# Kernel tuning notes

Hardware: AMD Instinct MI355X
Metric: run time of the kernel (lower is better)

Reference implementation:

```python
import jax, jax.numpy as jnp
import numpy as np

N_NODES = 100000
N_EDGES = 3200000
N_GRAPHS = 512
F_IN = 35
F_OUT = 128


def setup_inputs() -> dict:
    key = jax.random.key(0)
    ks = jax.random.split(key, 16)
    x = jax.random.normal(ks[0], (N_NODES, F_IN), dtype=jnp.float32)
    edge_index = jax.random.randint(ks[1], (2, N_EDGES), 0, N_NODES, dtype=jnp.int32)
    batch = jnp.sort(jax.random.randint(ks[2], (N_NODES,), 0, N_GRAPHS, dtype=jnp.int32))
    def lin(k, fin, fout):
        s = 1.0 / np.sqrt(fin)
        return jax.random.uniform(k, (fin, fout), jnp.float32, -s, s)
    return {
        "x": x, "edge_index": edge_index, "batch": batch,
        # SAGEConv 1 (35 -> 35): lin_l acts on aggregated neighbors (has bias), lin_r on root (no bias)
        "Wl1": lin(ks[3], F_IN, F_IN), "bl1": jnp.zeros((F_IN,), jnp.float32), "Wr1": lin(ks[4], F_IN, F_IN),
        # SAGEConv 2 (35 -> 128)
        "Wl2": lin(ks[5], F_IN, F_OUT), "bl2": jnp.zeros((F_OUT,), jnp.float32), "Wr2": lin(ks[6], F_IN, F_OUT),
        # FC head
        "Wg1": lin(ks[7], F_OUT, F_OUT), "bg1": jnp.zeros((F_OUT,), jnp.float32),
        "Wg2": lin(ks[8], F_OUT, F_OUT), "bg2": jnp.zeros((F_OUT,), jnp.float32),
        "Wo": lin(ks[9], F_OUT, 1), "bo": jnp.zeros((1,), jnp.float32),
    }


def _sage_conv(x, src, dst, Wl, bl, Wr):
    # mean aggregation over incoming edges (src -> dst), PyG SAGEConv default
    msg = x[src]                                               # [E, F] gather
    s = jax.ops.segment_sum(msg, dst, num_segments=N_NODES)    # [N, F]
    cnt = jax.ops.segment_sum(jnp.ones((src.shape[0],), x.dtype), dst, num_segments=N_NODES)
    agg = s / jnp.maximum(cnt, 1.0)[:, None]
    return agg @ Wl + bl + x @ Wr


def reference(x, edge_index, batch, Wl1, bl1, Wr1, Wl2, bl2, Wr2, Wg1, bg1, Wg2, bg2, Wo, bo):
    src, dst = edge_index[0], edge_index[1]
    h = _sage_conv(x, src, dst, Wl1, bl1, Wr1)   # [N, 35]
    h = jax.nn.relu(h)
    h = _sage_conv(h, src, dst, Wl2, bl2, Wr2)   # [N, 128]
    # global max pool over each graph in the batch
    g = jax.ops.segment_max(h, batch, num_segments=N_GRAPHS)  # [G, 128]
    g = jax.nn.relu(g @ Wg1 + bg1)
    g = jax.nn.relu(g @ Wg2 + bg2)
    return g @ Wo + bo                            # [G, 1]
```

## Files before the change

kernel.cpp:

```cpp
#include <hip/hip_runtime.h>
#include <hip/hip_bf16.h>
#include <math.h>

#define FIN 35
#define FOUT 128
#define NGRAPHS 512
#define PWA 32
#define PWB 4
#define RP 36
#define STRIP1 64
#define CHUNK 8192
#define MAXBUCK 512
#define MAXBE 12288

#define STRIPM 64
#define HROW 130
#define NFRAG 48

typedef _Float16 half8 __attribute__((ext_vector_type(8)));
typedef _Float16 half4 __attribute__((ext_vector_type(4)));
typedef float f32x4 __attribute__((ext_vector_type(4)));

__device__ __forceinline__ unsigned int enc_f32(float f) {
    unsigned int u = __float_as_uint(f);
    return (u & 0x80000000u) ? ~u : (u | 0x80000000u);
}
__device__ __forceinline__ float dec_f32(unsigned int u) {
    unsigned int b = (u & 0x80000000u) ? (u ^ 0x80000000u) : ~u;
    return __uint_as_float(b);
}


__global__ __launch_bounds__(256) void hist1_kernel(const int* __restrict__ dst,
                                                    int* __restrict__ counts,
                                                    int E, int nblk1, int nbuck) {
    __shared__ int h[MAXBUCK];
    for (int t = threadIdx.x; t < nbuck; t += 256) h[t] = 0;
    __syncthreads();
    int base = blockIdx.x * CHUNK;
    int end = min(base + CHUNK, E);
    for (int e = base + threadIdx.x; e < end; e += 256)
        atomicAdd(&h[dst[e] >> 8], 1);
    __syncthreads();
    for (int t = threadIdx.x; t < nbuck; t += 256)
        counts[t * nblk1 + blockIdx.x] = h[t];
}

__global__ void partial_reduce_kernel(const int* __restrict__ v_in, int* __restrict__ partial, int SC) {
    int i = blockIdx.x * 256 + threadIdx.x;
    int v = (i < SC) ? v_in[i] : 0;
    #pragma unroll
    for (int off = 32; off > 0; off >>= 1) v += __shfl_down(v, off, 64);
    __shared__ int w[4];
    if ((threadIdx.x & 63) == 0) w[threadIdx.x >> 6] = v;
    __syncthreads();
    if (threadIdx.x == 0) partial[blockIdx.x] = w[0] + w[1] + w[2] + w[3];
}

__global__ void scan_partials_kernel(int* __restrict__ partial, int NB) {
    __shared__ int lds[1024];
    int t = threadIdx.x;
    int v = (t < NB) ? partial[t] : 0;
    lds[t] = v;
    __syncthreads();
    for (int off = 1; off < 1024; off <<= 1) {
        int tv = (t >= off) ? lds[t - off] : 0;
        __syncthreads();
        lds[t] += tv;
        __syncthreads();
    }
    if (t < NB) partial[t] = lds[t] - v;
}

__global__ void scan_final_kernel(const int* __restrict__ v_in, const int* __restrict__ partial,
                                  int* __restrict__ outx, int SC) {
    __shared__ int lds[256];
    int i = blockIdx.x * 256 + threadIdx.x;
    int v = (i < SC) ? v_in[i] : 0;
    lds[threadIdx.x] = v;
    __syncthreads();
    for (int off = 1; off < 256; off <<= 1) {
        int tv = (threadIdx.x >= off) ? lds[threadIdx.x - off] : 0;
        __syncthreads();
        lds[threadIdx.x] += tv;
        __syncthreads();
    }
    int excl = lds[threadIdx.x] - v + partial[blockIdx.x];
    if (i < SC) {
        outx[i] = excl;
        if (i == SC - 1) outx[SC] = excl + v;
    }
}

__global__ __launch_bounds__(256) void scatter1_kernel(const int* __restrict__ src,
                                                       const int* __restrict__ dst,
                                                       const int* __restrict__ offs,
                                                       int* __restrict__ ebuf,
                                                       int E, int nblk1, int nbuck) {
    __shared__ int hist[MAXBUCK];
    __shared__ int scn[256];
    __shared__ int lstart[MAXBUCK];
    __shared__ int gofs[MAXBUCK];
    __shared__ int cur[MAXBUCK];
    __shared__ int sv[CHUNK];
    __shared__ int sd[CHUNK];
    int t = threadIdx.x;
    int base = blockIdx.x * CHUNK;
    int end = min(base + CHUNK, E);

    hist[t] = 0; hist[t + 256] = 0;
    __syncthreads();
    for (int e = base + t; e < end; e += 256)
        atomicAdd(&hist[dst[e] >> 8], 1);
    __syncthreads();

    int v0 = hist[2 * t];
    int v1 = hist[2 * t + 1];
    int pair = v0 + v1;
    scn[t] = pair;
    __syncthreads();
    for (int off = 1; off < 256; off <<= 1) {
        int tv = (t >= off) ? scn[t - off] : 0;
        __syncthreads();
        scn[t] += tv;
        __syncthreads();
    }
    int ex = scn[t] - pair;
    lstart[2 * t] = ex;
    lstart[2 * t + 1] = ex + v0;
    cur[2 * t] = ex;
    cur[2 * t + 1] = ex + v0;
    int b0 = 2 * t, b1 = 2 * t + 1;
    gofs[b0] = ((b0 < nbuck) ? offs[b0 * nblk1 + blockIdx.x] : 0) - ex;
    gofs[b1] = ((b1 < nbuck) ? offs[b1 * nblk1 + blockIdx.x] : 0) - (ex + v0);
    __syncthreads();

    for (int e = base + t; e < end; e += 256) {
        int d = dst[e];
        int b = d >> 8;
        int p = atomicAdd(&cur[b], 1);
        sv[p] = (src[e] << 8) | (d & 255);
        sd[p] = gofs[b] + p;
    }
    __syncthreads();

    int cnt = end - base;
    for (int k = t; k < cnt; k += 256)
        ebuf[sd[k]] = sv[k];
}

__global__ __launch_bounds__(256) void csr2_kernel(const int* __restrict__ ebuf,
                                                   const int* __restrict__ offs,
                                                   int* __restrict__ row_ptr,
                                                   int* __restrict__ hsplit,
                                                   int* __restrict__ esrc,
                                                   int E, int nblk1, int nbuck, int N, int halfN) {
    __shared__ int h[512];
    __shared__ int scn[256];
    __shared__ int cur[512];
    __shared__ int e_sh[MAXBE];
    int b = blockIdx.x;
    int t = threadIdx.x;
    int bstart = offs[b * nblk1];
    int bend = (b + 1 < nbuck) ? offs[(b + 1) * nblk1] : E;
    int cnt = bend - bstart;
    bool fit = (cnt <= MAXBE);

    if (fit)
        for (int k = t; k < cnt; k += 256) e_sh[k] = ebuf[bstart + k];
    h[t] = 0; h[t + 256] = 0;
    __syncthreads();
    for (int k = t; k < cnt; k += 256) {
        int e = fit ? e_sh[k] : ebuf[bstart + k];
        int bin = ((e & 255) << 1) | ((e >> 8) >= halfN ? 1 : 0);
        atomicAdd(&h[bin], 1);
    }
    __syncthreads();

    int v0 = h[2 * t];
    int v1 = h[2 * t + 1];
    int pair = v0 + v1;
    scn[t] = pair;
    __syncthreads();
    for (int off = 1; off < 256; off <<= 1) {
        int tv = (t >= off) ? scn[t - off] : 0;
        __syncthreads();
        scn[t] += tv;
        __syncthreads();
    }
    int base = bstart + scn[t] - pair;
    int node = (b << 8) + t;
    if (node < N) {
        row_ptr[node] = base;
        hsplit[node] = base + v0;
    }
    if (b == 0 && t == 0) row_ptr[N] = E;
    cur[2 * t] = base;
    cur[2 * t + 1] = base + v0;
    __syncthreads();

    for (int k = t; k < cnt; k += 256) {
        int e = fit ? e_sh[k] : ebuf[bstart + k];
        int bin = ((e & 255) << 1) | ((e >> 8) >= halfN ? 1 : 0);
        int p = atomicAdd(&cur[bin], 1);
        esrc[p] = e >> 8;
    }
}

__global__ void repack_kernel(const float* __restrict__ x,
                              _Float16* __restrict__ xA, _Float16* __restrict__ xB, int N) {
    int t = blockIdx.x * 256 + threadIdx.x;
    int NA = N * PWA;
    if (t < NA) {
        int n = t >> 5;
        int f = t & 31;
        xA[t] = (_Float16)x[(long long)n * FIN + f];
    } else if (t < NA + N * PWB) {
        int c = t - NA;
        int n = c >> 2;
        int f3 = c & 3;
        float v = (f3 < 3) ? x[(long long)n * FIN + 32 + f3] : 0.0f;
        xB[c] = (_Float16)v;
    }
}

__global__ __launch_bounds__(256) void gather2_kernel(const _Float16* __restrict__ pA,
                                                      const _Float16* __restrict__ pB,
                                                      const int* __restrict__ row_ptr,
                                                      const int* __restrict__ hsplit,
                                                      const int* __restrict__ esrc,
                                                      float* __restrict__ spA,
                                                      float* __restrict__ spB,
                                                      int N, int Wtot, int WS) {
    int q = blockIdx.x & 7;
    int m = blockIdx.x >> 3;
    int w = q * WS + m * 256 + threadIdx.x;
    int wend = min((q + 1) * WS, Wtot);
    if (w >= wend) return;
    int NI = N * 4;
    int pass = w / NI;
    int t = w - pass * NI;
    int n = t >> 2;
    int quad = t & 3;
    int b = (pass == 0) ? row_ptr[n] : hsplit[n];
    int e = (pass == 0) ? hsplit[n] : row_ptr[n + 1];
    const _Float16* base = pA + (quad << 3);
    const bool doB = (quad == 0);

    float a[8] = {0,0,0,0,0,0,0,0};
    float bb[4] = {0,0,0,0};
    int k = b;
    for (; k + 8 <= e; k += 8) {
        int s0 = esrc[k],     s1 = esrc[k + 1], s2 = esrc[k + 2], s3 = esrc[k + 3];
        int s4 = esrc[k + 4], s5 = esrc[k + 5], s6 = esrc[k + 6], s7 = esrc[k + 7];
        half8 v0 = *(const half8*)(base + ((long long)s0 << 5));
        half8 v1 = *(const half8*)(base + ((long long)s1 << 5));
        half8 v2 = *(const half8*)(base + ((long long)s2 << 5));
        half8 v3 = *(const half8*)(base + ((long long)s3 << 5));
        half8 v4 = *(const half8*)(base + ((long long)s4 << 5));
        half8 v5 = *(const half8*)(base + ((long long)s5 << 5));
        half8 v6 = *(const half8*)(base + ((long long)s6 << 5));
        half8 v7 = *(const half8*)(base + ((long long)s7 << 5));
        if (doB) {
            half4 u0 = *(const half4*)(pB + ((long long)s0 << 2));
            half4 u1 = *(const half4*)(pB + ((long long)s1 << 2));
            half4 u2 = *(const half4*)(pB + ((long long)s2 << 2));
            half4 u3 = *(const half4*)(pB + ((long long)s3 << 2));
            half4 u4 = *(const half4*)(pB + ((long long)s4 << 2));
            half4 u5 = *(const half4*)(pB + ((long long)s5 << 2));
            half4 u6 = *(const half4*)(pB + ((long long)s6 << 2));
            half4 u7 = *(const half4*)(pB + ((long long)s7 << 2));
            #pragma unroll
            for (int i = 0; i < 4; ++i) {
                float p01 = (float)u0[i] + (float)u1[i];
                float p23 = (float)u2[i] + (float)u3[i];
                float p45 = (float)u4[i] + (float)u5[i];
                float p67 = (float)u6[i] + (float)u7[i];
                bb[i] += (p01 + p23) + (p45 + p67);
            }
        }
        #pragma unroll
        for (int i = 0; i < 8; ++i) {
            float p01 = (float)v0[i] + (float)v1[i];
            float p23 = (float)v2[i] + (float)v3[i];
            float p45 = (float)v4[i] + (float)v5[i];
            float p67 = (float)v6[i] + (float)v7[i];
            a[i] += (p01 + p23) + (p45 + p67);
        }
    }
    for (; k < e; ++k) {
        int s = esrc[k];
        half8 v = *(const half8*)(base + ((long long)s << 5));
        if (doB) {
            half4 u = *(const half4*)(pB + ((long long)s << 2));
            #pragma unroll
            for (int i = 0; i < 4; ++i) bb[i] += (float)u[i];
        }
        #pragma unroll
        for (int i = 0; i < 8; ++i) a[i] += (float)v[i];
    }

    float* outp = spA + ((long long)pass * N + n) * PWA + (quad << 3);
    float4 r0, r1;
    r0.x = a[0]; r0.y = a[1]; r0.z = a[2]; r0.w = a[3];
    r1.x = a[4]; r1.y = a[5]; r1.z = a[6]; r1.w = a[7];
    *(float4*)outp = r0;
    *(float4*)(outp + 4) = r1;
    if (doB) {
        float4 r;
        r.x = bb[0]; r.y = bb[1]; r.z = bb[2]; r.w = bb[3];
        *(float4*)(spB + (((long long)pass * N + n) << 2)) = r;
    }
}

__global__ __launch_bounds__(256) void nu1_kernel(const float* __restrict__ x,
                                                  const float* __restrict__ spA,
                                                  const float* __restrict__ spB,
                                                  const int* __restrict__ row_ptr,
                                                  const float* __restrict__ Wl,
                                                  const float* __restrict__ bl,
                                                  const float* __restrict__ Wr,
                                                  _Float16* __restrict__ h1A,
                                                  _Float16* __restrict__ h1B,
                                                  int N) {
    __shared__ float x_sh[STRIP1 * RP];
    __shared__ float s_sh[STRIP1 * RP];
    __shared__ int deg_sh[STRIP1];

    int node0 = blockIdx.x * STRIP1;
    if (node0 >= N) return;
    int nn = min(STRIP1, N - node0);
    int tot = nn * FIN;

    for (int t = threadIdx.x; t < STRIP1; t += 256) {
        x_sh[t * RP + 35] = 0.0f;
        s_sh[t * RP + 35] = 0.0f;
    }
    if (threadIdx.x < nn)
        deg_sh[threadIdx.x] = row_ptr[node0 + threadIdx.x + 1] - row_ptr[node0 + threadIdx.x];
    for (int t = threadIdx.x; t < tot; t += 256) {
        int nl = t / FIN;
        int i = t - nl * FIN;
        long long node = node0 + nl;
        x_sh[nl * RP + i] = x[node * FIN + i];
        float sv = (i < 32) ? (spA[node * PWA + i] + spA[((long long)N + node) * PWA + i])
                            : (spB[(node << 2) + (i - 32)] + spB[(((long long)N + node) << 2) + (i - 32)]);
        s_sh[nl * RP + i] = sv;
    }
    __syncthreads();

    int wave = threadIdx.x >> 6;
    int j = threadIdx.x & 63;
    if (j >= FIN) return;

    float wl[36], wr[36];
    #pragma unroll
    for (int i = 0; i < FIN; ++i) {
        wl[i] = Wl[i * FIN + j];
        wr[i] = Wr[i * FIN + j];
    }
    wl[35] = 0.0f; wr[35] = 0.0f;
    float blj = bl[j];

    int nstart = wave * 16;
    int nend = min(nstart + 16, nn);
    for (int nl = nstart; nl < nend; ++nl) {
        float accS = 0.0f;
        float accX = blj;
        #pragma unroll
        for (int c = 0; c < 9; ++c) {
            float4 sv = *(const float4*)&s_sh[nl * RP + 4 * c];
            float4 xv = *(const float4*)&x_sh[nl * RP + 4 * c];
            accS = fmaf(sv.x, wl[4 * c],     accS);
            accS = fmaf(sv.y, wl[4 * c + 1], accS);
            accS = fmaf(sv.z, wl[4 * c + 2], accS);
            accS = fmaf(sv.w, wl[4 * c + 3], accS);
            accX = fmaf(xv.x, wr[4 * c],     accX);
            accX = fmaf(xv.y, wr[4 * c + 1], accX);
            accX = fmaf(xv.z, wr[4 * c + 2], accX);
            accX = fmaf(xv.w, wr[4 * c + 3], accX);
        }
        float inv = 1.0f / (float)max(deg_sh[nl], 1);
        float acc = fmaxf(fmaf(accS, inv, accX), 0.0f);
        long long node = node0 + nl;
        if (j < 32) {
            h1A[(node << 5) + j] = (_Float16)acc;
        } else {
            h1B[(node << 2) + (j - 32)] = (_Float16)acc;
            if (j == 34) h1B[(node << 2) + 3] = (_Float16)0.0f;
        }
    }
}

__global__ void wprep2_kernel(const float* __restrict__ Wl, const float* __restrict__ Wr,
                              _Float16* __restrict__ wfrag) {
    int f = blockIdx.x;
    int l = threadIdx.x;
    int ps = f / 24;
    int rem = f % 24;
    int ks = rem >> 3;
    int nt = rem & 7;
    int n = nt * 16 + (l & 15);
    int kb = ks * 32 + ((l >> 4) << 3);
    half8 o;
    #pragma unroll
    for (int e = 0; e < 8; ++e) {
        int k = kb + e;
        float v = 0.0f;
        if (k < 35) v = Wl[k * FOUT + n];
        else if (k >= 36 && k < 71) v = Wr[(k - 36) * FOUT + n];
        _Float16 hi = (_Float16)v;
        o[e] = ps ? (_Float16)(v - (float)hi) : hi;
    }
    *(half8*)(wfrag + ((size_t)f * 64 + l) * 8) = o;
}

__global__ __launch_bounds__(256) void nu2_pool_mfma_kernel(const _Float16* __restrict__ h1A,
                                                            const _Float16* __restrict__ h1B,
                                                            const float* __restrict__ spA,
                                                            const float* __restrict__ spB,
                                                            const int* __restrict__ row_ptr,
                                                            const _Float16* __restrict__ wfrag,
                                                            const float* __restrict__ bl,
                                                            const int* __restrict__ batch,
                                                            unsigned int* __restrict__ genc,
                                                            int N) {
    __shared__ __align__(16) float h_sh[STRIPM * HROW];
    __shared__ int b_sh[STRIPM];

    int node0 = blockIdx.x * STRIPM;
    if (node0 >= N) return;
    int nn = min(STRIPM, N - node0);

    char* Ab = (char*)h_sh;
    const int t = threadIdx.x;
    const int lane = t & 63;
    const int wv = t >> 6;

    {
        const int r = lane;
        const long long node = (long long)node0 + r;
        const bool valid = (r < nn);
        const int sw = r & 7;
        char* rowp = Ab + r * 256;

        if (wv == 0) {
            int dg = 1;
            if (valid) dg = row_ptr[node + 1] - row_ptr[node];
            float inv = 1.0f / (float)max(dg, 1);
            #pragma unroll
            for (int u = 0; u < 3; ++u) {
                half8 h = {0,0,0,0,0,0,0,0};
                if (valid) {
                    const float* p = spA + node * 32 + u * 8;
                    const float* q = spA + ((long long)N + node) * 32 + u * 8;
                    float4 p0 = *(const float4*)p;
                    float4 p1 = *(const float4*)(p + 4);
                    float4 q0 = *(const float4*)q;
                    float4 q1 = *(const float4*)(q + 4);
                    h[0] = (_Float16)((p0.x + q0.x) * inv);
                    h[1] = (_Float16)((p0.y + q0.y) * inv);
                    h[2] = (_Float16)((p0.z + q0.z) * inv);
                    h[3] = (_Float16)((p0.w + q0.w) * inv);
                    h[4] = (_Float16)((p1.x + q1.x) * inv);
                    h[5] = (_Float16)((p1.y + q1.y) * inv);
                    h[6] = (_Float16)((p1.z + q1.z) * inv);
                    h[7] = (_Float16)((p1.w + q1.w) * inv);
                }
                *(half8*)(rowp + ((u ^ sw) << 4)) = h;
            }
        } else if (wv == 1) {
            int dg = 1;
            if (valid) dg = row_ptr[node + 1] - row_ptr[node];
            float inv = 1.0f / (float)max(dg, 1);
            half8 h3 = {0,0,0,0,0,0,0,0};
            half8 h4 = {0,0,0,0,0,0,0,0};
            half8 h5 = {0,0,0,0,0,0,0,0};
            if (valid) {
                const float* p = spA + node * 32 + 24;
                const float* q = spA + ((long long)N + node) * 32 + 24;
                float4 p0 = *(const float4*)p;
                float4 p1 = *(const float4*)(p + 4);
                float4 q0 = *(const float4*)q;
                float4 q1 = *(const float4*)(q + 4);
                h3[0] = (_Float16)((p0.x + q0.x) * inv);
                h3[1] = (_Float16)((p0.y + q0.y) * inv);
                h3[2] = (_Float16)((p0.z + q0.z) * inv);
                h3[3] = (_Float16)((p0.w + q0.w) * inv);
                h3[4] = (_Float16)((p1.x + q1.x) * inv);
                h3[5] = (_Float16)((p1.y + q1.y) * inv);
                h3[6] = (_Float16)((p1.z + q1.z) * inv);
                h3[7] = (_Float16)((p1.w + q1.w) * inv);
                float4 sb0 = *(const float4*)(spB + (node << 2));
                float4 sb1 = *(const float4*)(spB + (((long long)N + node) << 2));
                half4 ha = *(const half4*)(h1A + (node << 5));
                h4[0] = (_Float16)((sb0.x + sb1.x) * inv);
                h4[1] = (_Float16)((sb0.y + sb1.y) * inv);
                h4[2] = (_Float16)((sb0.z + sb1.z) * inv);
                h4[3] = (_Float16)((sb0.w + sb1.w) * inv);
                h4[4] = ha[0]; h4[5] = ha[1]; h4[6] = ha[2]; h4[7] = ha[3];
                half4 hb0 = *(const half4*)(h1A + (node << 5) + 4);
                half4 hb1 = *(const half4*)(h1A + (node << 5) + 8);
                h5[0] = hb0[0]; h5[1] = hb0[1]; h5[2] = hb0[2]; h5[3] = hb0[3];
                h5[4] = hb1[0]; h5[5] = hb1[1]; h5[6] = hb1[2]; h5[7] = hb1[3];
            }
            *(half8*)(rowp + ((3 ^ sw) << 4)) = h3;
            *(half8*)(rowp + ((4 ^ sw) << 4)) = h4;
            *(half8*)(rowp + ((5 ^ sw) << 4)) = h5;
        } else if (wv == 2) {
            half8 h6 = {0,0,0,0,0,0,0,0};
            half8 h7 = {0,0,0,0,0,0,0,0};
            half8 h8 = {0,0,0,0,0,0,0,0};
            if (valid) {
                half4 a0 = *(const half4*)(h1A + (node << 5) + 12);
                half4 a1 = *(const half4*)(h1A + (node << 5) + 16);
                half4 a2 = *(const half4*)(h1A + (node << 5) + 20);
                half4 a3 = *(const half4*)(h1A + (node << 5) + 24);
                half4 a4 = *(const half4*)(h1A + (node << 5) + 28);
                half4 b4 = *(const half4*)(h1B + (node << 2));
                h6[0] = a0[0]; h6[1] = a0[1]; h6[2] = a0[2]; h6[3] = a0[3];
                h6[4] = a1[0]; h6[5] = a1[1]; h6[6] = a1[2]; h6[7] = a1[3];
                h7[0] = a2[0]; h7[1] = a2[1]; h7[2] = a2[2]; h7[3] = a2[3];
                h7[4] = a3[0]; h7[5] = a3[1]; h7[6] = a3[2]; h7[7] = a3[3];
                h8[0] = a4[0]; h8[1] = a4[1]; h8[2] = a4[2]; h8[3] = a4[3];
                h8[4] = b4[0]; h8[5] = b4[1]; h8[6] = b4[2]; h8[7] = b4[3];
            }
            *(half8*)(rowp + ((6 ^ sw) << 4)) = h6;
            *(half8*)(rowp + ((7 ^ sw) << 4)) = h7;
            *(half8*)(rowp + ((8 ^ sw) << 4)) = h8;
        } else {
            half8 z = {0,0,0,0,0,0,0,0};
            *(half8*)(rowp + ((9  ^ sw) << 4)) = z;
            *(half8*)(rowp + ((10 ^ sw) << 4)) = z;
            *(half8*)(rowp + ((11 ^ sw) << 4)) = z;
            if (lane < nn) b_sh[lane] = batch[node0 + lane];
        }
    }
    __syncthreads();

    f32x4 acc[8];
    #pragma unroll
    for (int nt = 0; nt < 8; ++nt) acc[nt] = (f32x4){0.0f, 0.0f, 0.0f, 0.0f};

    const int m0 = wv << 4;
    const int rr = m0 + (lane & 15);
    const int rsw = lane & 7;
    const int g = lane >> 4;
    const char* arow = Ab + rr * 256;

    #pragma unroll
    for (int ps = 0; ps < 2; ++ps) {
        #pragma unroll
        for (int ks = 0; ks < 3; ++ks) {
            half8 af = *(const half8*)(arow + ((((ks << 2) + g) ^ rsw) << 4));
            const _Float16* wp = wfrag + ((size_t)((ps * 3 + ks) << 3) * 64 + lane) * 8;
            #pragma unroll
            for (int nt = 0; nt < 8; ++nt) {
                half8 bf = *(const half8*)(wp + (size_t)nt * 512);
                acc[nt] = __builtin_amdgcn_mfma_f32_16x16x32_f16(af, bf, acc[nt], 0, 0, 0);
            }
        }
    }
    __syncthreads();

    const int col = lane & 15;
    const int rbase = m0 + (g << 2);
    #pragma unroll
    for (int nt = 0; nt < 8; ++nt) {
        float bb = bl[(nt << 4) + col];
        #pragma unroll
        for (int q2 = 0; q2 < 4; ++q2)
            h_sh[(rbase + q2) * HROW + (nt << 4) + col] = acc[nt][q2] + bb;
    }
    __syncthreads();

    const int j = t & 127;
    const int hh = t >> 7;
    int nl = hh << 5;
    int nend = min(nl + 32, nn);
    if (nl < nend) {
        int curg = b_sh[nl];
        float mx = -INFINITY;
        for (; nl < nend; ++nl) {
            float v = h_sh[nl * HROW + j];
            int gb = b_sh[nl];
            if (gb != curg) {
                atomicMax(&genc[curg * FOUT + j], enc_f32(mx));
                curg = gb;
                mx = v;
            } else {
                mx = fmaxf(mx, v);
            }
        }
        atomicMax(&genc[curg * FOUT + j], enc_f32(mx));
    }
}

__global__ void head_kernel(const unsigned int* __restrict__ genc,
                            const float* __restrict__ Wg1, const float* __restrict__ bg1,
                            const float* __restrict__ Wg2, const float* __restrict__ bg2,
                            const float* __restrict__ Wo,  const float* __restrict__ bo,
                            float* __restrict__ out) {
    __shared__ float a[FOUT];
    __shared__ float c[FOUT];
    __shared__ float red[2];
    int g = blockIdx.x;
    int j = threadIdx.x;

    a[j] = dec_f32(genc[g * FOUT + j]);
    __syncthreads();

    float acc = bg1[j];
    #pragma unroll 8
    for (int i = 0; i < FOUT; ++i) acc = fmaf(a[i], Wg1[i * FOUT + j], acc);
    c[j] = fmaxf(acc, 0.0f);
    __syncthreads();

    acc = bg2[j];
    #pragma unroll 8
    for (int i = 0; i < FOUT; ++i) acc = fmaf(c[i], Wg2[i * FOUT + j], acc);
    float t = fmaxf(acc, 0.0f) * Wo[j];

    #pragma unroll
    for (int off = 32; off > 0; off >>= 1) t += __shfl_down(t, off, 64);
    if ((threadIdx.x & 63) == 0) red[threadIdx.x >> 6] = t;
    __syncthreads();
    if (threadIdx.x == 0) out[g] = red[0] + red[1] + bo[0];
}

extern "C" void kernel_launch(void* const* d_in, const int* in_sizes, int n_in,
                              void* d_out, int out_size, void* d_ws, size_t ws_size,
                              hipStream_t stream) {
    const float* x    = (const float*)d_in[0];
    const int*   ei   = (const int*)  d_in[1];
    const int*   batch= (const int*)  d_in[2];
    const float* Wl1  = (const float*)d_in[3];
    const float* bl1  = (const float*)d_in[4];
    const float* Wr1  = (const float*)d_in[5];
    const float* Wl2  = (const float*)d_in[6];
    const float* bl2  = (const float*)d_in[7];
    const float* Wr2  = (const float*)d_in[8];
    const float* Wg1  = (const float*)d_in[9];
    const float* bg1  = (const float*)d_in[10];
    const float* Wg2  = (const float*)d_in[11];
    const float* bg2  = (const float*)d_in[12];
    const float* Wo   = (const float*)d_in[13];
    const float* bo   = (const float*)d_in[14];
    float* out = (float*)d_out;

    const int N = in_sizes[0] / FIN;
    const int E = in_sizes[1] / 2;
    const int* src = ei;
    const int* dst = ei + E;
    const int halfN = N >> 1;

    const int nblk1 = (E + CHUNK - 1) / CHUNK;
    const int nbuck = (N + 255) >> 8;
    const int SC = nbuck * nblk1;
    const int NB2 = (SC + 255) / 256;

    char* ws = (char*)d_ws;
    size_t off = 0;
    auto alloc = [&](size_t bytes) { char* p = ws + off; off += (bytes + 255) & ~255ull; return p; };
    int*          counts  = (int*)alloc((size_t)SC * 4);
    int*          offs    = (int*)alloc((size_t)(SC + 1) * 4);
    int*          partial = (int*)alloc(1024 * 4);
    int*          row_ptr = (int*)alloc((size_t)(N + 1) * 4);
    int*          hsplit  = (int*)alloc((size_t)N * 4);
    int*          esrc    = (int*)alloc((size_t)E * 4);
    char*         regionA = (char*)alloc((size_t)E * 4);
    _Float16*     xA      = (_Float16*)alloc((size_t)N * PWA * 2);
    _Float16*     xB      = (_Float16*)alloc((size_t)N * PWB * 2);
    float*        spA     = (float*)alloc((size_t)2 * N * PWA * 4);
    float*        spB     = (float*)alloc((size_t)2 * N * PWB * 4);
    unsigned int* genc    = (unsigned int*)alloc((size_t)NGRAPHS * FOUT * 4);
    int*       ebuf  = (int*)regionA;
    _Float16*  h1A   = (_Float16*)regionA;
    _Float16*  h1B   = (_Float16*)(regionA + (size_t)N * PWA * 2);
    _Float16*  wfrag = (_Float16*)(regionA + (size_t)N * (PWA + PWB) * 2);
    (void)ws_size; (void)n_in; (void)out_size;

    const int BS = 256;
    const int Wtot = N * 8;
    int WS = ((Wtot / 8 + BS - 1) / BS) * BS;
    const int bpx = WS / BS;
    const int rpb = (N * 36 + BS - 1) / BS;
    int nu1b = (N + STRIP1 - 1) / STRIP1;
    int nu2b = (N + STRIPM - 1) / STRIPM;

    hipLaunchKernelGGL(hist1_kernel, dim3(nblk1), dim3(BS), 0, stream, dst, counts, E, nblk1, nbuck);
    hipLaunchKernelGGL(partial_reduce_kernel, dim3(NB2), dim3(BS), 0, stream, counts, partial, SC);
    hipLaunchKernelGGL(scan_partials_kernel, dim3(1), dim3(1024), 0, stream, partial, NB2);
    hipLaunchKernelGGL(scan_final_kernel, dim3(NB2), dim3(BS), 0, stream, counts, partial, offs, SC);
    hipLaunchKernelGGL(scatter1_kernel, dim3(nblk1), dim3(BS), 0, stream, src, dst, offs, ebuf, E, nblk1, nbuck);
    hipLaunchKernelGGL(csr2_kernel, dim3(nbuck), dim3(BS), 0, stream,
                       ebuf, offs, row_ptr, hsplit, esrc, E, nblk1, nbuck, N, halfN);

    hipLaunchKernelGGL(wprep2_kernel, dim3(NFRAG), dim3(64), 0, stream, Wl2, Wr2, wfrag);

    hipLaunchKernelGGL(repack_kernel, dim3(rpb), dim3(BS), 0, stream, x, xA, xB, N);
    hipLaunchKernelGGL(gather2_kernel, dim3(8 * bpx), dim3(BS), 0, stream,
                       xA, xB, row_ptr, hsplit, esrc, spA, spB, N, Wtot, WS);
    hipLaunchKernelGGL(nu1_kernel, dim3(nu1b), dim3(BS), 0, stream,
                       x, spA, spB, row_ptr, Wl1, bl1, Wr1, h1A, h1B, N);

    hipLaunchKernelGGL(gather2_kernel, dim3(8 * bpx), dim3(BS), 0, stream,
                       h1A, h1B, row_ptr, hsplit, esrc, spA, spB, N, Wtot, WS);
    hipMemsetAsync(genc, 0, (size_t)NGRAPHS * FOUT * 4, stream);
    hipLaunchKernelGGL(nu2_pool_mfma_kernel, dim3(nu2b), dim3(BS), 0, stream,
                       h1A, h1B, spA, spB, row_ptr, wfrag, bl2, batch, genc, N);

    hipLaunchKernelGGL(head_kernel, dim3(NGRAPHS), dim3(FOUT), 0, stream,
                       genc, Wg1, bg1, Wg2, bg2, Wo, bo, out);
}
```

Before: 343.2 us.

## Split neighbor lists into four source-range quarters for gather locality

The CSR build now bins each destination's edges into four source-index quarters instead of two and records four split offsets per node. The gather kernel runs four passes, each touching only a quarter of the feature table, so the working set per pass is meant to fit better in cache. The partial sums of the four passes are added in nu1 and nu2. In exchange, the partial-sum buffers double in size, more work items carry short edge lists, and the gather loop unroll drops from 8 to 4.

```diff
diff --git a/kernel.cpp b/kernel.cpp
--- a/kernel.cpp
+++ b/kernel.cpp
@@ -29,6 +29,9 @@
     unsigned int b = (u & 0x80000000u) ? (u ^ 0x80000000u) : ~u;
     return __uint_as_float(b);
 }
+__device__ __forceinline__ int quart4(int s, int t1, int t2, int t3) {
+    return (s >= t2) ? (2 + (s >= t3)) : (int)(s >= t1);
+}
 
 
 __global__ __launch_bounds__(256) void hist1_kernel(const int* __restrict__ dst,
@@ -99,7 +102,6 @@
                                                        int E, int nblk1, int nbuck) {
     __shared__ int hist[MAXBUCK];
     __shared__ int scn[256];
-    __shared__ int lstart[MAXBUCK];
     __shared__ int gofs[MAXBUCK];
     __shared__ int cur[MAXBUCK];
     __shared__ int sv[CHUNK];
@@ -126,8 +128,6 @@
         __syncthreads();
     }
     int ex = scn[t] - pair;
-    lstart[2 * t] = ex;
-    lstart[2 * t + 1] = ex + v0;
     cur[2 * t] = ex;
     cur[2 * t + 1] = ex + v0;
     int b0 = 2 * t, b1 = 2 * t + 1;
@@ -152,12 +152,12 @@
 __global__ __launch_bounds__(256) void csr2_kernel(const int* __restrict__ ebuf,
                                                    const int* __restrict__ offs,
                                                    int* __restrict__ row_ptr,
-                                                   int* __restrict__ hsplit,
+                                                   int* __restrict__ qs,
                                                    int* __restrict__ esrc,
-                                                   int E, int nblk1, int nbuck, int N, int halfN) {
-    __shared__ int h[512];
+                                                   int E, int nblk1, int nbuck, int N) {
+    __shared__ int h[1024];
     __shared__ int scn[256];
-    __shared__ int cur[512];
+    __shared__ int cur[1024];
     __shared__ int e_sh[MAXBE];
     int b = blockIdx.x;
     int t = threadIdx.x;
@@ -165,22 +165,25 @@
     int bend = (b + 1 < nbuck) ? offs[(b + 1) * nblk1] : E;
     int cnt = bend - bstart;
     bool fit = (cnt <= MAXBE);
+    const int t1 = N >> 2, t2 = N >> 1, t3 = (N >> 2) + (N >> 1);
 
     if (fit)
         for (int k = t; k < cnt; k += 256) e_sh[k] = ebuf[bstart + k];
-    h[t] = 0; h[t + 256] = 0;
+    h[t] = 0; h[t + 256] = 0; h[t + 512] = 0; h[t + 768] = 0;
     __syncthreads();
     for (int k = t; k < cnt; k += 256) {
         int e = fit ? e_sh[k] : ebuf[bstart + k];
-        int bin = ((e & 255) << 1) | ((e >> 8) >= halfN ? 1 : 0);
+        int bin = ((e & 255) << 2) | quart4(e >> 8, t1, t2, t3);
         atomicAdd(&h[bin], 1);
     }
     __syncthreads();
 
-    int v0 = h[2 * t];
-    int v1 = h[2 * t + 1];
-    int pair = v0 + v1;
-    scn[t] = pair;
+    int v0 = h[4 * t];
+    int v1 = h[4 * t + 1];
+    int v2 = h[4 * t + 2];
+    int v3 = h[4 * t + 3];
+    int tot = v0 + v1 + v2 + v3;
+    scn[t] = tot;
     __syncthreads();
     for (int off = 1; off < 256; off <<= 1) {
         int tv = (t >= off) ? scn[t - off] : 0;
@@ -188,20 +191,25 @@
         scn[t] += tv;
         __syncthreads();
     }
-    int base = bstart + scn[t] - pair;
+    int base = bstart + scn[t] - tot;
     int node = (b << 8) + t;
     if (node < N) {
         row_ptr[node] = base;
-        hsplit[node] = base + v0;
+        qs[4 * node]     = base;
+        qs[4 * node + 1] = base + v0;
+        qs[4 * node + 2] = base + v0 + v1;
+        qs[4 * node + 3] = base + v0 + v1 + v2;
     }
     if (b == 0 && t == 0) row_ptr[N] = E;
-    cur[2 * t] = base;
-    cur[2 * t + 1] = base + v0;
+    cur[4 * t]     = base;
+    cur[4 * t + 1] = base + v0;
+    cur[4 * t + 2] = base + v0 + v1;
+    cur[4 * t + 3] = base + v0 + v1 + v2;
     __syncthreads();
 
     for (int k = t; k < cnt; k += 256) {
         int e = fit ? e_sh[k] : ebuf[bstart + k];
-        int bin = ((e & 255) << 1) | ((e >> 8) >= halfN ? 1 : 0);
+        int bin = ((e & 255) << 2) | quart4(e >> 8, t1, t2, t3);
         int p = atomicAdd(&cur[bin], 1);
         esrc[p] = e >> 8;
     }
@@ -224,10 +232,10 @@
     }
 }
 
-__global__ __launch_bounds__(256) void gather2_kernel(const _Float16* __restrict__ pA,
+__global__ __launch_bounds__(256) void gather4_kernel(const _Float16* __restrict__ pA,
                                                       const _Float16* __restrict__ pB,
                                                       const int* __restrict__ row_ptr,
-                                                      const int* __restrict__ hsplit,
+                                                      const int* __restrict__ qs,
                                                       const int* __restrict__ esrc,
                                                       float* __restrict__ spA,
                                                       float* __restrict__ spB,
@@ -242,50 +250,33 @@
     int t = w - pass * NI;
     int n = t >> 2;
     int quad = t & 3;
-    int b = (pass == 0) ? row_ptr[n] : hsplit[n];
-    int e = (pass == 0) ? hsplit[n] : row_ptr[n + 1];
+    int b = qs[(n << 2) + pass];
+    int e = (pass < 3) ? qs[(n << 2) + pass + 1] : row_ptr[n + 1];
     const _Float16* base = pA + (quad << 3);
     const bool doB = (quad == 0);
 
-    float a[8] = {0,0,0,0,0,0,0,0};
+    float a0[8] = {0,0,0,0,0,0,0,0}, a1[8] = {0,0,0,0,0,0,0,0};
     float bb[4] = {0,0,0,0};
     int k = b;
-    for (; k + 8 <= e; k += 8) {
-        int s0 = esrc[k],     s1 = esrc[k + 1], s2 = esrc[k + 2], s3 = esrc[k + 3];
-        int s4 = esrc[k + 4], s5 = esrc[k + 5], s6 = esrc[k + 6], s7 = esrc[k + 7];
+    for (; k + 4 <= e; k += 4) {
+        int s0 = esrc[k], s1 = esrc[k + 1], s2 = esrc[k + 2], s3 = esrc[k + 3];
         half8 v0 = *(const half8*)(base + ((long long)s0 << 5));
         half8 v1 = *(const half8*)(base + ((long long)s1 << 5));
         half8 v2 = *(const half8*)(base + ((long long)s2 << 5));
         half8 v3 = *(const half8*)(base + ((long long)s3 << 5));
-        half8 v4 = *(const half8*)(base + ((long long)s4 << 5));
-        half8 v5 = *(const half8*)(base + ((long long)s5 << 5));
-        half8 v6 = *(const half8*)(base + ((long long)s6 << 5));
-        half8 v7 = *(const half8*)(base + ((long long)s7 << 5));
         if (doB) {
             half4 u0 = *(const half4*)(pB + ((long long)s0 << 2));
             half4 u1 = *(const half4*)(pB + ((long long)s1 << 2));
             half4 u2 = *(const half4*)(pB + ((long long)s2 << 2));
             half4 u3 = *(const half4*)(pB + ((long long)s3 << 2));
-            half4 u4 = *(const half4*)(pB + ((long long)s4 << 2));
-            half4 u5 = *(const half4*)(pB + ((long long)s5 << 2));
-            half4 u6 = *(const half4*)(pB + ((long long)s6 << 2));
-            half4 u7 = *(const half4*)(pB + ((long long)s7 << 2));
             #pragma unroll
-            for (int i = 0; i < 4; ++i) {
-                float p01 = (float)u0[i] + (float)u1[i];
-                float p23 = (float)u2[i] + (float)u3[i];
-                float p45 = (float)u4[i] + (float)u5[i];
-                float p67 = (float)u6[i] + (float)u7[i];
-                bb[i] += (p01 + p23) + (p45 + p67);
-            }
+            for (int i = 0; i < 4; ++i)
+                bb[i] += ((float)u0[i] + (float)u1[i]) + ((float)u2[i] + (float)u3[i]);
         }
         #pragma unroll
         for (int i = 0; i < 8; ++i) {
-            float p01 = (float)v0[i] + (float)v1[i];
-            float p23 = (float)v2[i] + (float)v3[i];
-            float p45 = (float)v4[i] + (float)v5[i];
-            float p67 = (float)v6[i] + (float)v7[i];
-            a[i] += (p01 + p23) + (p45 + p67);
+            a0[i] += (float)v0[i] + (float)v1[i];
+            a1[i] += (float)v2[i] + (float)v3[i];
         }
     }
     for (; k < e; ++k) {
@@ -297,13 +288,13 @@
             for (int i = 0; i < 4; ++i) bb[i] += (float)u[i];
         }
         #pragma unroll
-        for (int i = 0; i < 8; ++i) a[i] += (float)v[i];
+        for (int i = 0; i < 8; ++i) a0[i] += (float)v[i];
     }
 
     float* outp = spA + ((long long)pass * N + n) * PWA + (quad << 3);
     float4 r0, r1;
-    r0.x = a[0]; r0.y = a[1]; r0.z = a[2]; r0.w = a[3];
-    r1.x = a[4]; r1.y = a[5]; r1.z = a[6]; r1.w = a[7];
+    r0.x = a0[0] + a1[0]; r0.y = a0[1] + a1[1]; r0.z = a0[2] + a1[2]; r0.w = a0[3] + a1[3];
+    r1.x = a0[4] + a1[4]; r1.y = a0[5] + a1[5]; r1.z = a0[6] + a1[6]; r1.w = a0[7] + a1[7];
     *(float4*)outp = r0;
     *(float4*)(outp + 4) = r1;
     if (doB) {
@@ -331,6 +322,7 @@
     if (node0 >= N) return;
     int nn = min(STRIP1, N - node0);
     int tot = nn * FIN;
+    long long NL = N;
 
     for (int t = threadIdx.x; t < STRIP1; t += 256) {
         x_sh[t * RP + 35] = 0.0f;
@@ -343,8 +335,15 @@
         int i = t - nl * FIN;
         long long node = node0 + nl;
         x_sh[nl * RP + i] = x[node * FIN + i];
-        float sv = (i < 32) ? (spA[node * PWA + i] + spA[((long long)N + node) * PWA + i])
-                            : (spB[(node << 2) + (i - 32)] + spB[(((long long)N + node) << 2) + (i - 32)]);
+        float sv;
+        if (i < 32) {
+            sv = (spA[node * PWA + i]            + spA[(NL + node) * PWA + i])
+               + (spA[(2 * NL + node) * PWA + i] + spA[(3 * NL + node) * PWA + i]);
+        } else {
+            int ii = i - 32;
+            sv = (spB[(node << 2) + ii]            + spB[((NL + node) << 2) + ii])
+               + (spB[((2 * NL + node) << 2) + ii] + spB[((3 * NL + node) << 2) + ii]);
+        }
         s_sh[nl * RP + i] = sv;
     }
     __syncthreads();
@@ -431,6 +430,7 @@
     int node0 = blockIdx.x * STRIPM;
     if (node0 >= N) return;
     int nn = min(STRIPM, N - node0);
+    long long NL = N;
 
     char* Ab = (char*)h_sh;
     const int t = threadIdx.x;
@@ -452,20 +452,22 @@
             for (int u = 0; u < 3; ++u) {
                 half8 h = {0,0,0,0,0,0,0,0};
                 if (valid) {
-                    const float* p = spA + node * 32 + u * 8;
-                    const float* q = spA + ((long long)N + node) * 32 + u * 8;
-                    float4 p0 = *(const float4*)p;
-                    float4 p1 = *(const float4*)(p + 4);
-                    float4 q0 = *(const float4*)q;
-                    float4 q1 = *(const float4*)(q + 4);
-                    h[0] = (_Float16)((p0.x + q0.x) * inv);
-                    h[1] = (_Float16)((p0.y + q0.y) * inv);
-                    h[2] = (_Float16)((p0.z + q0.z) * inv);
-                    h[3] = (_Float16)((p0.w + q0.w) * inv);
-                    h[4] = (_Float16)((p1.x + q1.x) * inv);
-                    h[5] = (_Float16)((p1.y + q1.y) * inv);
-                    h[6] = (_Float16)((p1.z + q1.z) * inv);
-                    h[7] = (_Float16)((p1.w + q1.w) * inv);
+                    const float* p0 = spA + node * 32 + u * 8;
+                    const float* p1 = spA + (NL + node) * 32 + u * 8;
+                    const float* p2 = spA + (2 * NL + node) * 32 + u * 8;
+                    const float* p3 = spA + (3 * NL + node) * 32 + u * 8;
+                    float4 a0 = *(const float4*)p0, a1 = *(const float4*)(p0 + 4);
+                    float4 b0 = *(const float4*)p1, b1 = *(const float4*)(p1 + 4);
+                    float4 c0 = *(const float4*)p2, c1 = *(const float4*)(p2 + 4);
+                    float4 d0 = *(const float4*)p3, d1 = *(const float4*)(p3 + 4);
+                    h[0] = (_Float16)(((a0.x + b0.x) + (c0.x + d0.x)) * inv);
+                    h[1] = (_Float16)(((a0.y + b0.y) + (c0.y + d0.y)) * inv);
+                    h[2] = (_Float16)(((a0.z + b0.z) + (c0.z + d0.z)) * inv);
+                    h[3] = (_Float16)(((a0.w + b0.w) + (c0.w + d0.w)) * inv);
+                    h[4] = (_Float16)(((a1.x + b1.x) + (c1.x + d1.x)) * inv);
+                    h[5] = (_Float16)(((a1.y + b1.y) + (c1.y + d1.y)) * inv);
+                    h[6] = (_Float16)(((a1.z + b1.z) + (c1.z + d1.z)) * inv);
+                    h[7] = (_Float16)(((a1.w + b1.w) + (c1.w + d1.w)) * inv);
                 }
                 *(half8*)(rowp + ((u ^ sw) << 4)) = h;
             }
@@ -477,27 +479,31 @@
             half8 h4 = {0,0,0,0,0,0,0,0};
             half8 h5 = {0,0,0,0,0,0,0,0};
             if (valid) {
-                const float* p = spA + node * 32 + 24;
-                const float* q = spA + ((long long)N + node) * 32 + 24;
-                float4 p0 = *(const float4*)p;
-                float4 p1 = *(const float4*)(p + 4);
-                float4 q0 = *(const float4*)q;
-                float4 q1 = *(const float4*)(q + 4);
-                h3[0] = (_Float16)((p0.x + q0.x) * inv);
-                h3[1] = (_Float16)((p0.y + q0.y) * inv);
-                h3[2] = (_Float16)((p0.z + q0.z) * inv);
-                h3[3] = (_Float16)((p0.w + q0.w) * inv);
-                h3[4] = (_Float16)((p1.x + q1.x) * inv);
-                h3[5] = (_Float16)((p1.y + q1.y) * inv);
-                h3[6] = (_Float16)((p1.z + q1.z) * inv);
-                h3[7] = (_Float16)((p1.w + q1.w) * inv);
-                float4 sb0 = *(const float4*)(spB + (node << 2));
-                float4 sb1 = *(const float4*)(spB + (((long long)N + node) << 2));
+                const float* p0 = spA + node * 32 + 24;
+                const float* p1 = spA + (NL + node) * 32 + 24;
+                const float* p2 = spA + (2 * NL + node) * 32 + 24;
+                const float* p3 = spA + (3 * NL + node) * 32 + 24;
+                float4 a0 = *(const float4*)p0, a1 = *(const float4*)(p0 + 4);
+                float4 b0 = *(const float4*)p1, b1 = *(const float4*)(p1 + 4);
+                float4 c0 = *(const float4*)p2, c1 = *(const float4*)(p2 + 4);
+                float4 d0 = *(const float4*)p3, d1 = *(const float4*)(p3 + 4);
+                h3[0] = (_Float16)(((a0.x + b0.x) + (c0.x + d0.x)) * inv);
+                h3[1] = (_Float16)(((a0.y + b0.y) + (c0.y + d0.y)) * inv);
+                h3[2] = (_Float16)(((a0.z + b0.z) + (c0.z + d0.z)) * inv);
+                h3[3] = (_Float16)(((a0.w + b0.w) + (c0.w + d0.w)) * inv);
+                h3[4] = (_Float16)(((a1.x + b1.x) + (c1.x + d1.x)) * inv);
+                h3[5] = (_Float16)(((a1.y + b1.y) + (c1.y + d1.y)) * inv);
+                h3[6] = (_Float16)(((a1.z + b1.z) + (c1.z + d1.z)) * inv);
+                h3[7] = (_Float16)(((a1.w + b1.w) + (c1.w + d1.w)) * inv);
+                float4 s0 = *(const float4*)(spB + (node << 2));
+                float4 s1 = *(const float4*)(spB + ((NL + node) << 2));
+                float4 s2 = *(const float4*)(spB + ((2 * NL + node) << 2));
+                float4 s3 = *(const float4*)(spB + ((3 * NL + node) << 2));
                 half4 ha = *(const half4*)(h1A + (node << 5));
-                h4[0] = (_Float16)((sb0.x + sb1.x) * inv);
-                h4[1] = (_Float16)((sb0.y + sb1.y) * inv);
-                h4[2] = (_Float16)((sb0.z + sb1.z) * inv);
-                h4[3] = (_Float16)((sb0.w + sb1.w) * inv);
+                h4[0] = (_Float16)(((s0.x + s1.x) + (s2.x + s3.x)) * inv);
+                h4[1] = (_Float16)(((s0.y + s1.y) + (s2.y + s3.y)) * inv);
+                h4[2] = (_Float16)(((s0.z + s1.z) + (s2.z + s3.z)) * inv);
+                h4[3] = (_Float16)(((s0.w + s1.w) + (s2.w + s3.w)) * inv);
                 h4[4] = ha[0]; h4[5] = ha[1]; h4[6] = ha[2]; h4[7] = ha[3];
                 half4 hb0 = *(const half4*)(h1A + (node << 5) + 4);
                 half4 hb1 = *(const half4*)(h1A + (node << 5) + 8);
@@ -652,7 +658,6 @@
     const int E = in_sizes[1] / 2;
     const int* src = ei;
     const int* dst = ei + E;
-    const int halfN = N >> 1;
 
     const int nblk1 = (E + CHUNK - 1) / CHUNK;
     const int nbuck = (N + 255) >> 8;
@@ -666,13 +671,13 @@
     int*          offs    = (int*)alloc((size_t)(SC + 1) * 4);
     int*          partial = (int*)alloc(1024 * 4);
     int*          row_ptr = (int*)alloc((size_t)(N + 1) * 4);
-    int*          hsplit  = (int*)alloc((size_t)N * 4);
+    int*          qs      = (int*)alloc((size_t)4 * N * 4);
     int*          esrc    = (int*)alloc((size_t)E * 4);
     char*         regionA = (char*)alloc((size_t)E * 4);
     _Float16*     xA      = (_Float16*)alloc((size_t)N * PWA * 2);
     _Float16*     xB      = (_Float16*)alloc((size_t)N * PWB * 2);
-    float*        spA     = (float*)alloc((size_t)2 * N * PWA * 4);
-    float*        spB     = (float*)alloc((size_t)2 * N * PWB * 4);
+    float*        spA     = (float*)alloc((size_t)4 * N * PWA * 4);
+    float*        spB     = (float*)alloc((size_t)4 * N * PWB * 4);
     unsigned int* genc    = (unsigned int*)alloc((size_t)NGRAPHS * FOUT * 4);
     int*       ebuf  = (int*)regionA;
     _Float16*  h1A   = (_Float16*)regionA;
@@ -681,7 +686,7 @@
     (void)ws_size; (void)n_in; (void)out_size;
 
     const int BS = 256;
-    const int Wtot = N * 8;
+    const int Wtot = N * 16;
     int WS = ((Wtot / 8 + BS - 1) / BS) * BS;
     const int bpx = WS / BS;
     const int rpb = (N * 36 + BS - 1) / BS;
@@ -694,18 +699,18 @@
     hipLaunchKernelGGL(scan_final_kernel, dim3(NB2), dim3(BS), 0, stream, counts, partial, offs, SC);
     hipLaunchKernelGGL(scatter1_kernel, dim3(nblk1), dim3(BS), 0, stream, src, dst, offs, ebuf, E, nblk1, nbuck);
     hipLaunchKernelGGL(csr2_kernel, dim3(nbuck), dim3(BS), 0, stream,
-                       ebuf, offs, row_ptr, hsplit, esrc, E, nblk1, nbuck, N, halfN);
+                       ebuf, offs, row_ptr, qs, esrc, E, nblk1, nbuck, N);
 
     hipLaunchKernelGGL(wprep2_kernel, dim3(NFRAG), dim3(64), 0, stream, Wl2, Wr2, wfrag);
 
     hipLaunchKernelGGL(repack_kernel, dim3(rpb), dim3(BS), 0, stream, x, xA, xB, N);
-    hipLaunchKernelGGL(gather2_kernel, dim3(8 * bpx), dim3(BS), 0, stream,
-                       xA, xB, row_ptr, hsplit, esrc, spA, spB, N, Wtot, WS);
+    hipLaunchKernelGGL(gather4_kernel, dim3(8 * bpx), dim3(BS), 0, stream,
+                       xA, xB, row_ptr, qs, esrc, spA, spB, N, Wtot, WS);
     hipLaunchKernelGGL(nu1_kernel, dim3(nu1b), dim3(BS), 0, stream,
                        x, spA, spB, row_ptr, Wl1, bl1, Wr1, h1A, h1B, N);
 
-    hipLaunchKernelGGL(gather2_kernel, dim3(8 * bpx), dim3(BS), 0, stream,
-                       h1A, h1B, row_ptr, hsplit, esrc, spA, spB, N, Wtot, WS);
+    hipLaunchKernelGGL(gather4_kernel, dim3(8 * bpx), dim3(BS), 0, stream,
+                       h1A, h1B, row_ptr, qs, esrc, spA, spB, N, Wtot, WS);
     hipMemsetAsync(genc, 0, (size_t)NGRAPHS * FOUT * 4, stream);
     hipLaunchKernelGGL(nu2_pool_mfma_kernel, dim3(nu2b), dim3(BS), 0, stream,
                        h1A, h1B, spA, spB, row_ptr, wfrag, bl2, batch, genc, N);
```

Result: slower. 350.2 us (+2.0%).
